# Optimization experiments

Measured on AMD Instinct MI355X. Metric: run time of the kernel, lower is better.

The kernel has to match this reference:

```python
import jax, jax.numpy as jnp
import numpy as np

EPS = 1e-06

def _l2_norm(t):
    # normalize over channel dim (-2): einsum('bcn,bn->bcn', t, 1/||t||_{2,dim=-2})
    inv = 1.0 / jnp.linalg.norm(t, ord=2, axis=-2)  # (B, L)
    return t * inv[:, None, :]


def setup_inputs() -> dict:
    key = jax.random.key(0)
    ks = jax.random.split(key, 8)
    B, C, D = 16, 2048, 1024  # D == d_model == Length
    s = 1.0 / np.sqrt(D)
    return {
        "x": jax.random.normal(ks[0], (B, C, D), dtype=jnp.float32),
        "Wq": jax.random.normal(ks[1], (D, D), dtype=jnp.float32) * s,
        "bq": jnp.zeros((D,), dtype=jnp.float32),
        "Wk": jax.random.normal(ks[2], (D, D), dtype=jnp.float32) * s,
        "bk": jnp.zeros((D,), dtype=jnp.float32),
        "Wv": jax.random.normal(ks[3], (D, D), dtype=jnp.float32) * s,
        "bv": jnp.zeros((D,), dtype=jnp.float32),
        "gamma": jax.random.normal(ks[4], (1,), dtype=jnp.float32) * 0.1,
    }


def reference(x, Wq, bq, Wk, bk, Wv, bv, gamma):
    B, C, L = x.shape
    # Linear layers act on last dim (torch Linear: x @ W.T + b)
    Q = x @ Wq.T + bq            # (B, C, L)
    K = x @ Wk.T + bk            # (B, C, L)
    V = x @ Wv.T + bv            # (B, C, L)
    Q = jnp.transpose(_l2_norm(Q), (0, 2, 1))  # (B, L, C)
    K = _l2_norm(K)                            # (B, C, L)
    # tailor_sum: (B, L)
    tailor_sum = 1.0 / (L + jnp.einsum('bnc,bc->bn', Q, jnp.sum(K, axis=-1) + EPS))
    # value_sum: (B, C) broadcast over L
    value_sum = jnp.sum(V, axis=-1)[:, :, None]            # (B, C, 1)
    matrix = jnp.einsum('bmn,bcn->bmc', K, V)              # (B, C, C)
    matrix_sum = value_sum + jnp.einsum('bnm,bmc->bcn', Q, matrix)  # (B, C, L)
    weight_value = matrix_sum * tailor_sum[:, None, :]     # (B, C, L)
    return x + gamma * weight_value
```

## Files before the change

kernel.cpp:

```cpp
#include <hip/hip_runtime.h>
#include <cstdint>

#define DEV static __device__ __forceinline__

typedef __attribute__((ext_vector_type(4))) float f32x4;
typedef __attribute__((ext_vector_type(4))) float fl4;
typedef __attribute__((ext_vector_type(4))) unsigned short us4;
typedef __attribute__((ext_vector_type(8))) unsigned short us8;
typedef __attribute__((ext_vector_type(2))) long l2v;

DEV float b2f(unsigned short u) {
  union { unsigned int i; float f; } c; c.i = ((unsigned int)u) << 16; return c.f;
}
DEV unsigned short f2b(float f) {
  union { float f; unsigned int i; } c; c.f = f;
  unsigned int u = c.i;
  u += 0x7fffu + ((u >> 16) & 1u);
  return (unsigned short)(u >> 16);
}
DEV unsigned int f4_to_fp8x4(float a, float b, float c, float d) {
  int r = __builtin_amdgcn_cvt_pk_fp8_f32(a, b, 0, false);
  r = __builtin_amdgcn_cvt_pk_fp8_f32(c, d, r, true);
  return (unsigned int)r;
}
DEV unsigned char f2f8(float v) {
  return (unsigned char)__builtin_amdgcn_cvt_pk_fp8_f32(v, v, 0, false);
}

DEV void gload16(const void* g, void* l) {
  __builtin_amdgcn_global_load_lds(
      (const __attribute__((address_space(1))) unsigned int*)g,
      (__attribute__((address_space(3))) unsigned int*)l, 16, 0, 0);
}

DEV float red16(float v) {
  v += __shfl_xor(v, 1); v += __shfl_xor(v, 2);
  v += __shfl_xor(v, 4); v += __shfl_xor(v, 8);
  return v;
}
DEV float red4lk(float v) {
  v += __shfl_xor(v, 16); v += __shfl_xor(v, 32);
  return v;
}

__global__ __launch_bounds__(256) void k_xcast(const float* __restrict__ src,
                                               unsigned short* __restrict__ dh,
                                               unsigned char* __restrict__ d8, long n) {
  long i = ((long)blockIdx.x * 256 + threadIdx.x) * 4;
  if (i >= n) return;
  fl4 v = *(const fl4*)(src + i);
  us4 o;
  o[0] = f2b(v[0]); o[1] = f2b(v[1]); o[2] = f2b(v[2]); o[3] = f2b(v[3]);
  *(us4*)(dh + i) = o;
  *(unsigned int*)(d8 + i) = f4_to_fp8x4(v[0], v[1], v[2], v[3]);
}

__global__ __launch_bounds__(256) void k_wcast8(const float* __restrict__ wq,
                                                const float* __restrict__ wk,
                                                const float* __restrict__ wv,
                                                unsigned char* __restrict__ dst) {
  const long i = ((long)blockIdx.x * 256 + threadIdx.x) * 4;
  const int seg = (int)(i >> 20);
  const float* s = seg == 0 ? wq : (seg == 1 ? wk : wv);
  fl4 v = *(const fl4*)(s + (i & 1048575));
  *(unsigned int*)(dst + i) = f4_to_fp8x4(v[0], v[1], v[2], v[3]);
}

__global__ __launch_bounds__(256) void k_bias_cat(const float* __restrict__ bq,
                                                  const float* __restrict__ bk,
                                                  const float* __restrict__ bv,
                                                  float* __restrict__ o) {
  const int t = blockIdx.x * 256 + threadIdx.x;
  o[t] = t < 1024 ? bq[t] : (t < 2048 ? bk[t - 1024] : bv[t - 2048]);
}

__global__ __launch_bounds__(256) void k_norms_fin(const float* __restrict__ pq,
                                                   const float* __restrict__ pk,
                                                   float* __restrict__ invq, float* __restrict__ invk) {
  const int gid = blockIdx.x * 256 + threadIdx.x;
  invq[gid] = rsqrtf(pq[gid]);
  invk[gid] = rsqrtf(pk[gid]);
}

__global__ __launch_bounds__(256) void k_tailor_fin(const float* __restrict__ Srow,
                                                    const float* __restrict__ invq,
                                                    const float* __restrict__ qsum,
                                                    float* __restrict__ tailor) {
  const int gid = blockIdx.x * 256 + threadIdx.x;
  tailor[gid] = 1.0f / (1024.0f + Srow[gid] + 1e-6f * invq[gid] * qsum[gid]);
}

#define MFMA_FP8(A, B, C) __builtin_amdgcn_mfma_f32_16x16x32_fp8_fp8((A), (B), (C), 0, 0, 0)
#define SBAR   __builtin_amdgcn_s_barrier()

__global__ __launch_bounds__(1024, 4)
void k_g16qkv8(const unsigned char* __restrict__ A,
               const unsigned char* __restrict__ Bt,
               unsigned char* __restrict__ QT8, unsigned char* __restrict__ KT8,
               unsigned char* __restrict__ Vout8,
               int Kb,
               const float* __restrict__ bias,
               float* __restrict__ r1, float* __restrict__ r2,
               float* __restrict__ r3, float* __restrict__ r4) {
  __shared__ __align__(16) unsigned char LDSU[131072];

  const int tid = threadIdx.x;
  const int wv = tid >> 6, lane = tid & 63;
  const int wr = wv >> 2, wcn = wv & 3;
  const int l15 = lane & 15, lk = lane >> 4;

  const int nx = gridDim.x;
  const int nwg = nx * gridDim.y;
  const int lin = blockIdx.y * nx + blockIdx.x;
  const int cpx = nwg >> 3;
  const int wg = (lin & 7) * cpx + (lin >> 3);
  const int bn = wg % nx;
  const int bm = wg / nx;

  const unsigned char* Ab = A + (long)bm * 256 * Kb;
  const unsigned char* Bb = Bt + (long)bn * 256 * Kb;

  const int scsw = (tid & 3) ^ ((tid >> 3) & 3);
  const long gOff = (long)(tid >> 2) * Kb + (long)scsw * 16;
  const int ldsb = wv * 1024;

  const int rdsw = (lk ^ ((l15 >> 1) & 3)) * 16;
  const int abase = (wr * 64 + l15) * 64;
  const int bbase = (wcn * 64 + l15) * 64;

  f32x4 acc[4][4];
#pragma unroll
  for (int i = 0; i < 4; ++i)
#pragma unroll
    for (int j = 0; j < 4; ++j) acc[i][j] = (f32x4){0.f, 0.f, 0.f, 0.f};

#define STAGEQ(T, BUF)                                                        \
  {                                                                           \
    const long kb = (long)(T) * 64;                                           \
    gload16(Ab + kb + gOff, LDSU + (BUF) * 16384 + ldsb);                     \
    gload16(Bb + kb + gOff, LDSU + 65536 + (BUF) * 16384 + ldsb);             \
  }

  STAGEQ(0, 0)
  STAGEQ(1, 1)

  const int NT = Kb >> 6;
  for (int t = 0; t < NT; ++t) {
    if (t < NT - 1) { asm volatile("s_waitcnt vmcnt(2)" ::: "memory"); }
    else            { asm volatile("s_waitcnt vmcnt(0)" ::: "memory"); }
    if ((t & 1) == 0) SBAR;
    if (t + 2 < NT) STAGEQ(t + 2, (t + 2) & 3)

    const unsigned char* Asc = LDSU + (t & 3) * 16384;
    const unsigned char* Bsc = LDSU + 65536 + (t & 3) * 16384;
    l2v Bf[4], Af[4];
#pragma unroll
    for (int j = 0; j < 4; ++j)
      Bf[j] = *(const l2v*)&Bsc[bbase + j * 1024 + rdsw];
#pragma unroll
    for (int i = 0; i < 4; ++i)
      Af[i] = *(const l2v*)&Asc[abase + i * 1024 + rdsw];

    __builtin_amdgcn_s_setprio(1);
#pragma unroll
    for (int i = 0; i < 4; ++i)
#pragma unroll
      for (int j = 0; j < 4; ++j) {
        acc[i][j] = MFMA_FP8(Af[i][0], Bf[j][0], acc[i][j]);
        acc[i][j] = MFMA_FP8(Af[i][1], Bf[j][1], acc[i][j]);
      }
    __builtin_amdgcn_s_setprio(0);
  }
#undef STAGEQ
  SBAR;

  const int row0 = bm * 256 + wr * 64;
  const int col0 = bn * 256 + wcn * 64;

  const int seg = bn >> 2;
  const int b = bm >> 3;
  float bvj[4];
#pragma unroll
  for (int j = 0; j < 4; ++j) bvj[j] = bias[col0 + j * 16 + l15];
  const int colL0 = col0 & 1023;
  unsigned char* sc8 = LDSU;

  if (seg < 2) {
#pragma unroll
    for (int i = 0; i < 4; ++i)
#pragma unroll
      for (int j = 0; j < 4; ++j) {
        const int p = wcn * 64 + j * 16 + l15;
        const int m = wr * 64 + i * 16 + lk * 4;
        const unsigned int pk4 = f4_to_fp8x4(acc[i][j][0] + bvj[j], acc[i][j][1] + bvj[j],
                                             acc[i][j][2] + bvj[j], acc[i][j][3] + bvj[j]);
        *(unsigned int*)&sc8[p * 256 + (((m >> 4) ^ (p & 15)) << 4) + (m & 15)] = pk4;
      }
#pragma unroll
    for (int j = 0; j < 4; ++j) {
      const int colL = colL0 + j * 16 + l15;
      float ss = 0.f, sm = 0.f;
#pragma unroll
      for (int i = 0; i < 4; ++i)
#pragma unroll
        for (int r = 0; r < 4; ++r) {
          const float v = acc[i][j][r] + bvj[j];
          ss += v * v; sm += v;
        }
      ss = red4lk(ss);
      if (seg == 0) sm = red4lk(sm);
      if (lk == 0) {
        atomicAdd(&(seg == 0 ? r1 : r3)[(long)b * 1024 + colL], ss);
        if (seg == 0) atomicAdd(&r2[(long)b * 1024 + colL], sm);
      }
    }
    SBAR;
    unsigned char* tp = (seg == 0 ? QT8 : KT8) + (long)b * 2097152;
    const int P0 = (bn & 3) * 256;
    const int M0 = (bm & 7) * 256;
#pragma unroll
    for (int it = 0; it < 4; ++it) {
      const int p = it * 64 + (tid >> 4);
      const int c = tid & 15;
      us8 v = *(const us8*)&sc8[p * 256 + ((c ^ (p & 15)) << 4)];
      *(us8*)&tp[(long)(P0 + p) * 2048 + M0 + c * 16] = v;
    }
  } else {
#pragma unroll
    for (int i = 0; i < 4; ++i)
#pragma unroll
      for (int r = 0; r < 4; ++r) {
        const int rl = wr * 64 + i * 16 + lk * 4 + r;
        float sm = 0.f;
#pragma unroll
        for (int j = 0; j < 4; ++j) {
          const float v = acc[i][j][r] + bvj[j];
          sm += v;
          const int col = wcn * 64 + j * 16 + l15;
          sc8[rl * 256 + (((col >> 4) ^ (rl & 15)) << 4) + (col & 15)] = f2f8(v);
        }
        sm = red16(sm);
        if (l15 == 0) atomicAdd(&r4[row0 + i * 16 + lk * 4 + r], sm);
      }
    SBAR;
    const int C0 = (bn & 3) * 256;
#pragma unroll
    for (int it = 0; it < 4; ++it) {
      const int rl = it * 64 + (tid >> 4);
      const int c = tid & 15;
      us8 v = *(const us8*)&sc8[rl * 256 + ((c ^ (rl & 15)) << 4)];
      *(us8*)&Vout8[(long)(bm * 256 + rl) * 1024 + C0 + c * 16] = v;
    }
  }
}

template<int EPI>
__global__ __launch_bounds__(512)
void k_g8f8(const unsigned char* __restrict__ A,
            const unsigned char* __restrict__ Bt,
            void* __restrict__ O0,
            int Kb, long sA, long sB, long sC,
            float* __restrict__ r1, const float* __restrict__ r2,
            const float* __restrict__ r3,
            const unsigned short* __restrict__ xh,
            const float* __restrict__ Vsum,
            const float* __restrict__ tailor,
            const float* __restrict__ gptr) {
  __shared__ __align__(16) unsigned char LDSU[131072];

  const int tid = threadIdx.x;
  const int wv = tid >> 6, lane = tid & 63;
  const int wr = wv >> 2, wcn = wv & 3;
  const int l15 = lane & 15, lk = lane >> 4;

  const int nx = gridDim.x;
  const int nwg = nx * gridDim.y;
  const int lin = blockIdx.y * nx + blockIdx.x;
  const int cpx = nwg >> 3;
  const int wg = (lin & 7) * cpx + (lin >> 3);
  const int bn = wg % nx;
  const int bm = wg / nx;
  const int bz = blockIdx.z;

  const unsigned char* Ab = A + (long)bz * sA + (long)bm * 256 * Kb;
  const unsigned char* Bb = Bt + (long)bz * sB + (long)bn * 256 * Kb;

  const int scsw = (tid & 3) ^ ((tid >> 3) & 3);
  const long gOff = (long)(tid >> 2) * Kb + (long)scsw * 16;
  const int ldsb = wv * 1024;

  const int rdsw = (lk ^ ((l15 >> 1) & 3)) * 16;
  const int abase = (wr * 128 + l15) * 64;
  const int bbase = (wcn * 64 + l15) * 64;

  f32x4 acc[8][4];
#pragma unroll
  for (int i = 0; i < 8; ++i)
#pragma unroll
    for (int j = 0; j < 4; ++j) acc[i][j] = (f32x4){0.f, 0.f, 0.f, 0.f};

#define STAGES(T, BUF)                                                        \
  {                                                                           \
    const long kb = (long)(T) * 64;                                           \
    unsigned char* Asb = LDSU + (BUF) * 16384;                                \
    unsigned char* Bsb = LDSU + 65536 + (BUF) * 16384;                        \
    gload16(Ab + kb + gOff,              &Asb[ldsb]);                         \
    gload16(Ab + kb + gOff + 128L * Kb,  &Asb[8192 + ldsb]);                  \
    gload16(Bb + kb + gOff,              &Bsb[ldsb]);                         \
    gload16(Bb + kb + gOff + 128L * Kb,  &Bsb[8192 + ldsb]);                  \
  }

  STAGES(0, 0)
  STAGES(1, 1)

  const int NT = Kb >> 6;
  for (int t = 0; t < NT; ++t) {
    if (t < NT - 1) { asm volatile("s_waitcnt vmcnt(4)" ::: "memory"); }
    else            { asm volatile("s_waitcnt vmcnt(0)" ::: "memory"); }
    if ((t & 1) == 0) SBAR;
    if (t + 2 < NT) STAGES(t + 2, (t + 2) & 3)

    const unsigned char* Asc = LDSU + (t & 3) * 16384;
    const unsigned char* Bsc = LDSU + 65536 + (t & 3) * 16384;
    l2v Bf[4], Af[8];
#pragma unroll
    for (int j = 0; j < 4; ++j)
      Bf[j] = *(const l2v*)&Bsc[bbase + j * 1024 + rdsw];
#pragma unroll
    for (int i = 0; i < 8; ++i)
      Af[i] = *(const l2v*)&Asc[abase + i * 1024 + rdsw];

    __builtin_amdgcn_s_setprio(1);
#pragma unroll
    for (int i = 0; i < 8; ++i)
#pragma unroll
      for (int j = 0; j < 4; ++j) {
        acc[i][j] = MFMA_FP8(Af[i][0], Bf[j][0], acc[i][j]);
        acc[i][j] = MFMA_FP8(Af[i][1], Bf[j][1], acc[i][j]);
      }
    __builtin_amdgcn_s_setprio(0);
  }
#undef STAGES
  SBAR;

  const int row0 = bm * 256 + wr * 128;
  const int col0 = bn * 256 + wcn * 64;

  if constexpr (EPI == 4) {
    unsigned char* sc8 = LDSU;
    unsigned char* Cb = (unsigned char*)O0 + (long)bz * sC;
    float ivk[4];
#pragma unroll
    for (int j = 0; j < 4; ++j) ivk[j] = r3[bz * 1024 + col0 + j * 16 + l15];
#pragma unroll
    for (int i = 0; i < 8; ++i) {
      float ivq[4];
#pragma unroll
      for (int r = 0; r < 4; ++r) ivq[r] = r2[bz * 1024 + row0 + i * 16 + lk * 4 + r];
#pragma unroll
      for (int r = 0; r < 4; ++r) {
        const int rl = wr * 128 + i * 16 + lk * 4 + r;
        float sm = 0.f;
#pragma unroll
        for (int j = 0; j < 4; ++j) {
          const float v = acc[i][j][r] * ivq[r] * ivk[j];
          sm += v;
          const int col = wcn * 64 + j * 16 + l15;
          sc8[rl * 256 + (((col >> 4) ^ (rl & 15)) << 4) + (col & 15)] = f2f8(v);
        }
        sm = red16(sm);
        if (l15 == 0) atomicAdd(&r1[(long)bz * 1024 + row0 + i * 16 + lk * 4 + r], sm);
      }
    }
    SBAR;
#pragma unroll
    for (int it = 0; it < 8; ++it) {
      const int rl = it * 32 + (tid >> 4);
      const int c = tid & 15;
      us8 v = *(const us8*)&sc8[rl * 256 + ((c ^ (rl & 15)) << 4)];
      *(us8*)&Cb[(long)(bm * 256 + rl) * 1024 + bn * 256 + c * 16] = v;
    }
  } else {
    float* scf = (float*)LDSU;
    float* Cb = (float*)O0 + (long)bz * sC;
    const float g = gptr[0];
#pragma unroll
    for (int h = 0; h < 2; ++h) {
      if (wr == h) {
#pragma unroll
        for (int i = 0; i < 8; ++i)
#pragma unroll
          for (int j = 0; j < 4; ++j) {
            const int col = wcn * 64 + j * 16 + l15;
            const int cc = col >> 2, c3 = col & 3;
#pragma unroll
            for (int r = 0; r < 4; ++r) {
              const int rl = i * 16 + lk * 4 + r;
              scf[rl * 256 + ((cc ^ (rl & 15)) << 2) + c3] = acc[i][j][r];
            }
          }
      }
      SBAR;
#pragma unroll
      for (int it = 0; it < 16; ++it) {
        const int rl = it * 8 + wv;
        const int rg = bm * 256 + h * 128 + rl;
        const int c = lane;
        fl4 a4 = *(const fl4*)&scf[rl * 256 + ((c ^ (rl & 15)) << 2)];
        const int cg = bn * 256 + c * 4;
        us4 xv = *(const us4*)&xh[((long)bz * 2048 + rg) * 1024 + cg];
        fl4 tl = *(const fl4*)&tailor[bz * 1024 + cg];
        const float vs = Vsum[bz * 2048 + rg];
        fl4 o;
#pragma unroll
        for (int q = 0; q < 4; ++q) o[q] = b2f(xv[q]) + g * ((vs + a4[q]) * tl[q]);
        *(fl4*)&Cb[(long)rg * 1024 + cg] = o;
      }
      if (h == 0) SBAR;
    }
  }
}

extern "C" void kernel_launch(void* const* d_in, const int* in_sizes, int n_in,
                              void* d_out, int out_size, void* d_ws, size_t ws_size,
                              hipStream_t stream) {
  (void)in_sizes; (void)n_in; (void)out_size;
  const float* x     = (const float*)d_in[0];
  const float* Wq    = (const float*)d_in[1];
  const float* bq    = (const float*)d_in[2];
  const float* Wk    = (const float*)d_in[3];
  const float* bk    = (const float*)d_in[4];
  const float* Wv    = (const float*)d_in[5];
  const float* bv    = (const float*)d_in[6];
  const float* gamma = (const float*)d_in[7];

  const long NE = 16L * 2048 * 1024;

  char* w = (char*)d_ws;
  unsigned char*  QT8 = (unsigned char*)(w);
  unsigned char*  KT8 = (unsigned char*)(w + 33554432L);
  unsigned char*  V8  = (unsigned char*)(w + 67108864L);
  unsigned short* xh  = (unsigned short*)(w + 100663296L);
  unsigned char*  x8  = (unsigned char*)(w + 167772160L);
  unsigned char*  S8  = (unsigned char*)(w + 201326592L);
  size_t off = 218103808L;
  unsigned char* W8   = (unsigned char*)(w + off); off += 3145728;
  char* accbase = w + off;
  float* pq     = (float*)(w + off); off += 65536;
  float* qsum   = (float*)(w + off); off += 65536;
  float* pk     = (float*)(w + off); off += 65536;
  float* Vsum   = (float*)(w + off); off += 131072;
  float* Srow   = (float*)(w + off); off += 65536;
  const size_t accbytes = (size_t)(w + off - accbase);
  float* invq   = (float*)(w + off); off += 65536;
  float* invk   = (float*)(w + off); off += 65536;
  float* tailor = (float*)(w + off); off += 65536;
  float* bqkv   = (float*)(w + off); off += 12288;
  if (ws_size < off) return;

  hipMemsetAsync(accbase, 0, accbytes, stream);

  k_xcast<<<dim3((unsigned)(NE / 1024)), 256, 0, stream>>>(x, xh, x8, NE);
  k_wcast8<<<dim3(3072), 256, 0, stream>>>(Wq, Wk, Wv, W8);
  k_bias_cat<<<dim3(12), 256, 0, stream>>>(bq, bk, bv, bqkv);

  k_g16qkv8<<<dim3(12, 128, 1), 1024, 0, stream>>>(
      x8, W8, QT8, KT8, V8, 1024, bqkv, pq, qsum, pk, Vsum);

  k_norms_fin<<<dim3(64), 256, 0, stream>>>(pq, pk, invq, invk);

  k_g8f8<4><<<dim3(4, 4, 16), 512, 0, stream>>>(
      QT8, KT8, S8, 2048, 1024L * 2048, 1024L * 2048, 1024L * 1024,
      Srow, invq, invk, nullptr, nullptr, nullptr, nullptr);

  k_tailor_fin<<<dim3(64), 256, 0, stream>>>(Srow, invq, qsum, tailor);

  k_g8f8<1><<<dim3(4, 8, 16), 512, 0, stream>>>(
      V8, S8, d_out, 1024, 2048L * 1024, 1024L * 1024, 2048L * 1024,
      nullptr, nullptr, nullptr, xh, Vsum, tailor, gamma);
}
```

Measured before the change: 350.4 us.

## Fuse norm and tailor finalization into GEMMs and widen GEMM blocks to 16 waves

Removes the two small finalization kernels (inverse norms and tailor denominators) by computing rsqrt and the tailor reciprocal inline in the epilogues of the two downstream GEMMs. It also converts both 512-thread GEMM kernels into 1024-thread (16-wave) blocks where each wave owns a 64x64 tile instead of 128x64, halving per-wave accumulators and per-thread global loads per stage. The goal is to cut launch overhead and improve latency hiding. The cost is redundant rsqrt/divide work in the epilogue and more barriers in the output staging loop.

```diff
diff --git a/kernel.cpp b/kernel.cpp
--- a/kernel.cpp
+++ b/kernel.cpp
@@ -74,22 +74,6 @@
   o[t] = t < 1024 ? bq[t] : (t < 2048 ? bk[t - 1024] : bv[t - 2048]);
 }
 
-__global__ __launch_bounds__(256) void k_norms_fin(const float* __restrict__ pq,
-                                                   const float* __restrict__ pk,
-                                                   float* __restrict__ invq, float* __restrict__ invk) {
-  const int gid = blockIdx.x * 256 + threadIdx.x;
-  invq[gid] = rsqrtf(pq[gid]);
-  invk[gid] = rsqrtf(pk[gid]);
-}
-
-__global__ __launch_bounds__(256) void k_tailor_fin(const float* __restrict__ Srow,
-                                                    const float* __restrict__ invq,
-                                                    const float* __restrict__ qsum,
-                                                    float* __restrict__ tailor) {
-  const int gid = blockIdx.x * 256 + threadIdx.x;
-  tailor[gid] = 1.0f / (1024.0f + Srow[gid] + 1e-6f * invq[gid] * qsum[gid]);
-}
-
 #define MFMA_FP8(A, B, C) __builtin_amdgcn_mfma_f32_16x16x32_fp8_fp8((A), (B), (C), 0, 0, 0)
 #define SBAR   __builtin_amdgcn_s_barrier()
 
@@ -254,18 +238,13 @@
   }
 }
 
-template<int EPI>
-__global__ __launch_bounds__(512)
-void k_g8f8(const unsigned char* __restrict__ A,
-            const unsigned char* __restrict__ Bt,
-            void* __restrict__ O0,
-            int Kb, long sA, long sB, long sC,
-            float* __restrict__ r1, const float* __restrict__ r2,
-            const float* __restrict__ r3,
-            const unsigned short* __restrict__ xh,
-            const float* __restrict__ Vsum,
-            const float* __restrict__ tailor,
-            const float* __restrict__ gptr) {
+__global__ __launch_bounds__(1024, 4)
+void k_g16s8(const unsigned char* __restrict__ A,
+             const unsigned char* __restrict__ Bt,
+             unsigned char* __restrict__ Sout,
+             int Kb,
+             const float* __restrict__ pq, const float* __restrict__ pk,
+             float* __restrict__ Srow) {
   __shared__ __align__(16) unsigned char LDSU[131072];
 
   const int tid = threadIdx.x;
@@ -282,32 +261,28 @@
   const int bm = wg / nx;
   const int bz = blockIdx.z;
 
-  const unsigned char* Ab = A + (long)bz * sA + (long)bm * 256 * Kb;
-  const unsigned char* Bb = Bt + (long)bz * sB + (long)bn * 256 * Kb;
+  const unsigned char* Ab = A + (long)bz * 2097152 + (long)bm * 256 * Kb;
+  const unsigned char* Bb = Bt + (long)bz * 2097152 + (long)bn * 256 * Kb;
 
   const int scsw = (tid & 3) ^ ((tid >> 3) & 3);
   const long gOff = (long)(tid >> 2) * Kb + (long)scsw * 16;
   const int ldsb = wv * 1024;
 
   const int rdsw = (lk ^ ((l15 >> 1) & 3)) * 16;
-  const int abase = (wr * 128 + l15) * 64;
+  const int abase = (wr * 64 + l15) * 64;
   const int bbase = (wcn * 64 + l15) * 64;
 
-  f32x4 acc[8][4];
-#pragma unroll
-  for (int i = 0; i < 8; ++i)
+  f32x4 acc[4][4];
+#pragma unroll
+  for (int i = 0; i < 4; ++i)
 #pragma unroll
     for (int j = 0; j < 4; ++j) acc[i][j] = (f32x4){0.f, 0.f, 0.f, 0.f};
 
 #define STAGES(T, BUF)                                                        \
   {                                                                           \
     const long kb = (long)(T) * 64;                                           \
-    unsigned char* Asb = LDSU + (BUF) * 16384;                                \
-    unsigned char* Bsb = LDSU + 65536 + (BUF) * 16384;                        \
-    gload16(Ab + kb + gOff,              &Asb[ldsb]);                         \
-    gload16(Ab + kb + gOff + 128L * Kb,  &Asb[8192 + ldsb]);                  \
-    gload16(Bb + kb + gOff,              &Bsb[ldsb]);                         \
-    gload16(Bb + kb + gOff + 128L * Kb,  &Bsb[8192 + ldsb]);                  \
+    gload16(Ab + kb + gOff, LDSU + (BUF) * 16384 + ldsb);                     \
+    gload16(Bb + kb + gOff, LDSU + 65536 + (BUF) * 16384 + ldsb);             \
   }
 
   STAGES(0, 0)
@@ -315,24 +290,24 @@
 
   const int NT = Kb >> 6;
   for (int t = 0; t < NT; ++t) {
-    if (t < NT - 1) { asm volatile("s_waitcnt vmcnt(4)" ::: "memory"); }
+    if (t < NT - 1) { asm volatile("s_waitcnt vmcnt(2)" ::: "memory"); }
     else            { asm volatile("s_waitcnt vmcnt(0)" ::: "memory"); }
     if ((t & 1) == 0) SBAR;
     if (t + 2 < NT) STAGES(t + 2, (t + 2) & 3)
 
     const unsigned char* Asc = LDSU + (t & 3) * 16384;
     const unsigned char* Bsc = LDSU + 65536 + (t & 3) * 16384;
-    l2v Bf[4], Af[8];
+    l2v Bf[4], Af[4];
 #pragma unroll
     for (int j = 0; j < 4; ++j)
       Bf[j] = *(const l2v*)&Bsc[bbase + j * 1024 + rdsw];
 #pragma unroll
-    for (int i = 0; i < 8; ++i)
+    for (int i = 0; i < 4; ++i)
       Af[i] = *(const l2v*)&Asc[abase + i * 1024 + rdsw];
 
     __builtin_amdgcn_s_setprio(1);
 #pragma unroll
-    for (int i = 0; i < 8; ++i)
+    for (int i = 0; i < 4; ++i)
 #pragma unroll
       for (int j = 0; j < 4; ++j) {
         acc[i][j] = MFMA_FP8(Af[i][0], Bf[j][0], acc[i][j]);
@@ -343,81 +318,166 @@
 #undef STAGES
   SBAR;
 
-  const int row0 = bm * 256 + wr * 128;
+  const int row0 = bm * 256 + wr * 64;
   const int col0 = bn * 256 + wcn * 64;
-
-  if constexpr (EPI == 4) {
-    unsigned char* sc8 = LDSU;
-    unsigned char* Cb = (unsigned char*)O0 + (long)bz * sC;
-    float ivk[4];
-#pragma unroll
-    for (int j = 0; j < 4; ++j) ivk[j] = r3[bz * 1024 + col0 + j * 16 + l15];
-#pragma unroll
-    for (int i = 0; i < 8; ++i) {
-      float ivq[4];
-#pragma unroll
-      for (int r = 0; r < 4; ++r) ivq[r] = r2[bz * 1024 + row0 + i * 16 + lk * 4 + r];
-#pragma unroll
-      for (int r = 0; r < 4; ++r) {
-        const int rl = wr * 128 + i * 16 + lk * 4 + r;
-        float sm = 0.f;
+  unsigned char* sc8 = LDSU;
+
+  float ivk[4];
+#pragma unroll
+  for (int j = 0; j < 4; ++j) ivk[j] = rsqrtf(pk[bz * 1024 + col0 + j * 16 + l15]);
+#pragma unroll
+  for (int i = 0; i < 4; ++i)
+#pragma unroll
+    for (int r = 0; r < 4; ++r) {
+      const int rl = wr * 64 + i * 16 + lk * 4 + r;
+      const float ivq = rsqrtf(pq[bz * 1024 + row0 + i * 16 + lk * 4 + r]);
+      float sm = 0.f;
+#pragma unroll
+      for (int j = 0; j < 4; ++j) {
+        const float v = acc[i][j][r] * ivq * ivk[j];
+        sm += v;
+        const int col = wcn * 64 + j * 16 + l15;
+        sc8[rl * 256 + (((col >> 4) ^ (rl & 15)) << 4) + (col & 15)] = f2f8(v);
+      }
+      sm = red16(sm);
+      if (l15 == 0) atomicAdd(&Srow[(long)bz * 1024 + row0 + i * 16 + lk * 4 + r], sm);
+    }
+  SBAR;
+  unsigned char* Cb = Sout + (long)bz * 1048576;
+#pragma unroll
+  for (int it = 0; it < 4; ++it) {
+    const int rl = it * 64 + (tid >> 4);
+    const int c = tid & 15;
+    us8 v = *(const us8*)&sc8[rl * 256 + ((c ^ (rl & 15)) << 4)];
+    *(us8*)&Cb[(long)(bm * 256 + rl) * 1024 + bn * 256 + c * 16] = v;
+  }
+}
+
+__global__ __launch_bounds__(1024, 4)
+void k_g16fin(const unsigned char* __restrict__ A,
+              const unsigned char* __restrict__ Bt,
+              float* __restrict__ Out,
+              int Kb,
+              const unsigned short* __restrict__ xh,
+              const float* __restrict__ Vsum,
+              const float* __restrict__ Srow,
+              const float* __restrict__ pq,
+              const float* __restrict__ qsum,
+              const float* __restrict__ gptr) {
+  __shared__ __align__(16) unsigned char LDSU[131072];
+
+  const int tid = threadIdx.x;
+  const int wv = tid >> 6, lane = tid & 63;
+  const int wr = wv >> 2, wcn = wv & 3;
+  const int l15 = lane & 15, lk = lane >> 4;
+
+  const int nx = gridDim.x;
+  const int nwg = nx * gridDim.y;
+  const int lin = blockIdx.y * nx + blockIdx.x;
+  const int cpx = nwg >> 3;
+  const int wg = (lin & 7) * cpx + (lin >> 3);
+  const int bn = wg % nx;
+  const int bm = wg / nx;
+  const int bz = blockIdx.z;
+
+  const unsigned char* Ab = A + (long)bz * 2097152 + (long)bm * 256 * Kb;
+  const unsigned char* Bb = Bt + (long)bz * 1048576 + (long)bn * 256 * Kb;
+
+  const int scsw = (tid & 3) ^ ((tid >> 3) & 3);
+  const long gOff = (long)(tid >> 2) * Kb + (long)scsw * 16;
+  const int ldsb = wv * 1024;
+
+  const int rdsw = (lk ^ ((l15 >> 1) & 3)) * 16;
+  const int abase = (wr * 64 + l15) * 64;
+  const int bbase = (wcn * 64 + l15) * 64;
+
+  f32x4 acc[4][4];
+#pragma unroll
+  for (int i = 0; i < 4; ++i)
+#pragma unroll
+    for (int j = 0; j < 4; ++j) acc[i][j] = (f32x4){0.f, 0.f, 0.f, 0.f};
+
+#define STAGEF(T, BUF)                                                        \
+  {                                                                           \
+    const long kb = (long)(T) * 64;                                           \
+    gload16(Ab + kb + gOff, LDSU + (BUF) * 16384 + ldsb);                     \
+    gload16(Bb + kb + gOff, LDSU + 65536 + (BUF) * 16384 + ldsb);             \
+  }
+
+  STAGEF(0, 0)
+  STAGEF(1, 1)
+
+  const int NT = Kb >> 6;
+  for (int t = 0; t < NT; ++t) {
+    if (t < NT - 1) { asm volatile("s_waitcnt vmcnt(2)" ::: "memory"); }
+    else            { asm volatile("s_waitcnt vmcnt(0)" ::: "memory"); }
+    if ((t & 1) == 0) SBAR;
+    if (t + 2 < NT) STAGEF(t + 2, (t + 2) & 3)
+
+    const unsigned char* Asc = LDSU + (t & 3) * 16384;
+    const unsigned char* Bsc = LDSU + 65536 + (t & 3) * 16384;
+    l2v Bf[4], Af[4];
+#pragma unroll
+    for (int j = 0; j < 4; ++j)
+      Bf[j] = *(const l2v*)&Bsc[bbase + j * 1024 + rdsw];
+#pragma unroll
+    for (int i = 0; i < 4; ++i)
+      Af[i] = *(const l2v*)&Asc[abase + i * 1024 + rdsw];
+
+    __builtin_amdgcn_s_setprio(1);
+#pragma unroll
+    for (int i = 0; i < 4; ++i)
+#pragma unroll
+      for (int j = 0; j < 4; ++j) {
+        acc[i][j] = MFMA_FP8(Af[i][0], Bf[j][0], acc[i][j]);
+        acc[i][j] = MFMA_FP8(Af[i][1], Bf[j][1], acc[i][j]);
+      }
+    __builtin_amdgcn_s_setprio(0);
+  }
+#undef STAGEF
+  SBAR;
+
+  float* scf = (float*)LDSU;
+  float* Cb = Out + (long)bz * 2097152;
+  const float g = gptr[0];
+#pragma unroll
+  for (int h = 0; h < 4; ++h) {
+    if (wr == h) {
+#pragma unroll
+      for (int i = 0; i < 4; ++i)
 #pragma unroll
         for (int j = 0; j < 4; ++j) {
-          const float v = acc[i][j][r] * ivq[r] * ivk[j];
-          sm += v;
           const int col = wcn * 64 + j * 16 + l15;
-          sc8[rl * 256 + (((col >> 4) ^ (rl & 15)) << 4) + (col & 15)] = f2f8(v);
+          const int cc = col >> 2, c3 = col & 3;
+#pragma unroll
+          for (int r = 0; r < 4; ++r) {
+            const int rl = i * 16 + lk * 4 + r;
+            scf[rl * 256 + ((cc ^ (rl & 15)) << 2) + c3] = acc[i][j][r];
+          }
         }
-        sm = red16(sm);
-        if (l15 == 0) atomicAdd(&r1[(long)bz * 1024 + row0 + i * 16 + lk * 4 + r], sm);
-      }
     }
     SBAR;
 #pragma unroll
-    for (int it = 0; it < 8; ++it) {
-      const int rl = it * 32 + (tid >> 4);
-      const int c = tid & 15;
-      us8 v = *(const us8*)&sc8[rl * 256 + ((c ^ (rl & 15)) << 4)];
-      *(us8*)&Cb[(long)(bm * 256 + rl) * 1024 + bn * 256 + c * 16] = v;
+    for (int it = 0; it < 4; ++it) {
+      const int rl = it * 16 + wv;
+      const int rg = bm * 256 + h * 64 + rl;
+      const int c = lane;
+      fl4 a4 = *(const fl4*)&scf[rl * 256 + ((c ^ (rl & 15)) << 2)];
+      const int cg = bn * 256 + c * 4;
+      us4 xv = *(const us4*)&xh[((long)bz * 2048 + rg) * 1024 + cg];
+      fl4 sr = *(const fl4*)&Srow[bz * 1024 + cg];
+      fl4 pq4 = *(const fl4*)&pq[bz * 1024 + cg];
+      fl4 qs4 = *(const fl4*)&qsum[bz * 1024 + cg];
+      const float vs = Vsum[bz * 2048 + rg];
+      fl4 o;
+#pragma unroll
+      for (int q = 0; q < 4; ++q) {
+        const float tl = 1.0f / (1024.0f + sr[q] + 1e-6f * rsqrtf(pq4[q]) * qs4[q]);
+        o[q] = b2f(xv[q]) + g * ((vs + a4[q]) * tl);
+      }
+      *(fl4*)&Cb[(long)rg * 1024 + cg] = o;
     }
-  } else {
-    float* scf = (float*)LDSU;
-    float* Cb = (float*)O0 + (long)bz * sC;
-    const float g = gptr[0];
-#pragma unroll
-    for (int h = 0; h < 2; ++h) {
-      if (wr == h) {
-#pragma unroll
-        for (int i = 0; i < 8; ++i)
-#pragma unroll
-          for (int j = 0; j < 4; ++j) {
-            const int col = wcn * 64 + j * 16 + l15;
-            const int cc = col >> 2, c3 = col & 3;
-#pragma unroll
-            for (int r = 0; r < 4; ++r) {
-              const int rl = i * 16 + lk * 4 + r;
-              scf[rl * 256 + ((cc ^ (rl & 15)) << 2) + c3] = acc[i][j][r];
-            }
-          }
-      }
-      SBAR;
-#pragma unroll
-      for (int it = 0; it < 16; ++it) {
-        const int rl = it * 8 + wv;
-        const int rg = bm * 256 + h * 128 + rl;
-        const int c = lane;
-        fl4 a4 = *(const fl4*)&scf[rl * 256 + ((c ^ (rl & 15)) << 2)];
-        const int cg = bn * 256 + c * 4;
-        us4 xv = *(const us4*)&xh[((long)bz * 2048 + rg) * 1024 + cg];
-        fl4 tl = *(const fl4*)&tailor[bz * 1024 + cg];
-        const float vs = Vsum[bz * 2048 + rg];
-        fl4 o;
-#pragma unroll
-        for (int q = 0; q < 4; ++q) o[q] = b2f(xv[q]) + g * ((vs + a4[q]) * tl[q]);
-        *(fl4*)&Cb[(long)rg * 1024 + cg] = o;
-      }
-      if (h == 0) SBAR;
-    }
+    if (h < 3) SBAR;
   }
 }
 
@@ -452,9 +512,6 @@
   float* Vsum   = (float*)(w + off); off += 131072;
   float* Srow   = (float*)(w + off); off += 65536;
   const size_t accbytes = (size_t)(w + off - accbase);
-  float* invq   = (float*)(w + off); off += 65536;
-  float* invk   = (float*)(w + off); off += 65536;
-  float* tailor = (float*)(w + off); off += 65536;
   float* bqkv   = (float*)(w + off); off += 12288;
   if (ws_size < off) return;
 
@@ -467,15 +524,9 @@
   k_g16qkv8<<<dim3(12, 128, 1), 1024, 0, stream>>>(
       x8, W8, QT8, KT8, V8, 1024, bqkv, pq, qsum, pk, Vsum);
 
-  k_norms_fin<<<dim3(64), 256, 0, stream>>>(pq, pk, invq, invk);
-
-  k_g8f8<4><<<dim3(4, 4, 16), 512, 0, stream>>>(
-      QT8, KT8, S8, 2048, 1024L * 2048, 1024L * 2048, 1024L * 1024,
-      Srow, invq, invk, nullptr, nullptr, nullptr, nullptr);
-
-  k_tailor_fin<<<dim3(64), 256, 0, stream>>>(Srow, invq, qsum, tailor);
-
-  k_g8f8<1><<<dim3(4, 8, 16), 512, 0, stream>>>(
-      V8, S8, d_out, 1024, 2048L * 1024, 1024L * 1024, 2048L * 1024,
-      nullptr, nullptr, nullptr, xh, Vsum, tailor, gamma);
-}
+  k_g16s8<<<dim3(4, 4, 16), 1024, 0, stream>>>(
+      QT8, KT8, S8, 2048, pq, pk, Srow);
+
+  k_g16fin<<<dim3(4, 8, 16), 1024, 0, stream>>>(
+      V8, S8, (float*)d_out, 1024, xh, Vsum, Srow, pq, qsum, gamma);
+}
```

Measured after the change: 344.8 us (median of 2 runs). Within noise of the previous version (-1.6%).
